# Kernel tuning notes

Measured on AMD Instinct MI355X. Metric: run time of the kernel, lower is better.

The kernel has to match this reference:

```python
import jax, jax.numpy as jnp
import numpy as np

H = 256          # LSTM hidden size
P = 1            # proj_size
L = 5            # num LSTM layers
T = 1000         # sequence length (forced by Linear(1000, 100))


def _uniform(key, shape, scale):
    return jax.random.uniform(key, shape, dtype=jnp.float32, minval=-scale, maxval=scale)


def setup_inputs() -> dict:
    key = jax.random.key(0)
    ks = jax.random.split(key, 16)
    B = 128
    s = 1.0 / np.sqrt(H)  # PyTorch LSTM init scale
    inp = {
        "x": jax.random.normal(ks[0], (B, T, 1), dtype=jnp.float32),
        # stacked LSTM params: layer input dim is 1 for all layers (input_size=1, proj_size=1)
        "Wih": _uniform(ks[1], (L, 4 * H, 1), s),
        "Whh": _uniform(ks[2], (L, 4 * H, P), s),
        "bih": _uniform(ks[3], (L, 4 * H), s),
        "bhh": _uniform(ks[4], (L, 4 * H), s),
        "Whr": _uniform(ks[5], (L, P, H), s),
        # MLP head
        "W1": _uniform(ks[6], (100, 1000), 1.0 / np.sqrt(1000)),
        "b1": _uniform(ks[7], (100,), 1.0 / np.sqrt(1000)),
        "W2": _uniform(ks[8], (100, 100), 0.1),
        "b2": _uniform(ks[9], (100,), 0.1),
        "W3": _uniform(ks[10], (100, 100), 0.1),
        "b3": _uniform(ks[11], (100,), 0.1),
        "W4": _uniform(ks[12], (1, 100), 0.1),
        "b4": _uniform(ks[13], (1,), 0.1),
    }
    return inp


def _lstm_layer(x_seq, Wih, Whh, bih, bhh, Whr):
    """One projected LSTM layer. x_seq: [B, T, in_dim] -> [B, T, P]."""
    B = x_seq.shape[0]
    # precompute input contribution for all timesteps: [B, T, 4H]
    gx = jnp.einsum('bti,gi->btg', x_seq, Wih) + bih + bhh
    gx = jnp.transpose(gx, (1, 0, 2))  # [T, B, 4H] for scan

    def step(carry, g_t):
        h, c = carry                      # h: [B, P], c: [B, H]
        gates = g_t + h @ Whh.T           # [B, 4H]
        i = jax.nn.sigmoid(gates[:, 0 * H:1 * H])
        f = jax.nn.sigmoid(gates[:, 1 * H:2 * H])
        g = jnp.tanh(gates[:, 2 * H:3 * H])
        o = jax.nn.sigmoid(gates[:, 3 * H:4 * H])
        c = f * c + i * g
        h = (o * jnp.tanh(c)) @ Whr.T     # projected hidden: [B, P]
        return (h, c), h

    h0 = jnp.zeros((B, P), x_seq.dtype)
    c0 = jnp.zeros((B, H), x_seq.dtype)
    _, hs = jax.lax.scan(step, (h0, c0), gx)  # hs: [T, B, P]
    return jnp.transpose(hs, (1, 0, 2))       # [B, T, P]


def reference(x, Wih, Whh, bih, bhh, Whr, W1, b1, W2, b2, W3, b3, W4, b4):
    out = x
    for l in range(L):  # fixed 5 stacked layers
        out = _lstm_layer(out, Wih[l], Whh[l], bih[l], bhh[l], Whr[l])
    out = out[:, :, 0]                      # squeeze -> [B, 1000]
    out = jax.nn.sigmoid(out @ W1.T + b1)   # linear1 + Sigmoid
    out = jax.nn.sigmoid(out @ W2.T + b2)   # linear2 + Sigmoid
    out = jax.nn.relu(out @ W3.T + b3)      # linear3 + ReLU
    out = out @ W4.T + b4                   # linear4 -> [B, 1]
    return out
```

## Files before the change

### kernel.cpp

```cpp
#include <hip/hip_runtime.h>


#define LAYERS 5
#define TT 1000
#define BATCH 128
#define CH 40
#define NCH (TT / CH)

__device__ __forceinline__ float fast_exp2(float x) {
#if __has_builtin(__builtin_amdgcn_exp2f)
  return __builtin_amdgcn_exp2f(x);
#else
  return __exp2f(x);
#endif
}
__device__ __forceinline__ float fast_rcp(float x) {
#if __has_builtin(__builtin_amdgcn_rcpf)
  return __builtin_amdgcn_rcpf(x);
#else
  return 1.0f / x;
#endif
}
__device__ __forceinline__ float fast_sigmoid(float z) {
  float e = fast_exp2(-1.4426950408889634f * z);
  return fast_rcp(1.0f + e);
}
__device__ __forceinline__ float fast_tanh(float z) {
  float e = fast_exp2(-2.8853900817779268f * z);
  return fmaf(2.0f, fast_rcp(1.0f + e), -1.0f);
}

template <int CTRL>
__device__ __forceinline__ float dpp_add(float v) {
  int moved = __builtin_amdgcn_update_dpp(0, __builtin_bit_cast(int, v),
                                          CTRL, 0xF, 0xF, false);
  return v + __builtin_bit_cast(float, moved);
}

__device__ __forceinline__ float wave_sum(float v) {
  v = dpp_add<0x128>(v);
  v = dpp_add<0x124>(v);
  v = dpp_add<0x122>(v);
  v = dpp_add<0x121>(v);
  int sw = __builtin_amdgcn_ds_swizzle(__builtin_bit_cast(int, v), 0x401F);
  v = v + __builtin_bit_cast(float, sw);
  float lo = __builtin_bit_cast(float, __builtin_amdgcn_readlane(__builtin_bit_cast(int, v), 0));
  float hi = __builtin_bit_cast(float, __builtin_amdgcn_readlane(__builtin_bit_cast(int, v), 32));
  return lo + hi;
}

__device__ __forceinline__ float lane_bcast(float v, int s) {
  return __builtin_bit_cast(float, __builtin_amdgcn_readlane(__builtin_bit_cast(int, v), s));
}

__global__ __launch_bounds__(64) void lstm_wave_kernel(
    const float* __restrict__ x,
    const float* __restrict__ Wih,
    const float* __restrict__ Whh,
    const float* __restrict__ bih,
    const float* __restrict__ bhh,
    const float* __restrict__ Whr,
    float* __restrict__ seq,
    int* __restrict__ flags)
{
  const int bid  = blockIdx.x;
  const int l    = bid >> 7;
  const int b    = bid & 127;
  const int lane = threadIdx.x;

  float wi[4][4], wh[4][4], bs[4][4], whr[4], cc[4];
  const int base = l * 1024;
#pragma unroll
  for (int g = 0; g < 4; ++g)
#pragma unroll
    for (int k = 0; k < 4; ++k) {
      int j = base + g * 256 + k * 64 + lane;
      wi[g][k] = Wih[j];
      wh[g][k] = Whh[j];
      bs[g][k] = bih[j] + bhh[j];
    }
#pragma unroll
  for (int k = 0; k < 4; ++k) {
    whr[k] = Whr[l * 256 + k * 64 + lane];
    cc[k] = 0.0f;
  }

  const float* in  = (l == 0) ? (x + b * TT) : (seq + ((l - 1) * BATCH + b) * TT);
  float*       out = seq + (l * BATCH + b) * TT;
  int*       my_flag = flags + l * BATCH + b;
  const int* in_flag = (l > 0) ? (flags + (l - 1) * BATCH + b) : (const int*)flags;

  float h = 0.0f;
  for (int c = 0; c < NCH; ++c) {
    if (l > 0) {
      while (__hip_atomic_load(in_flag, __ATOMIC_ACQUIRE,
                               __HIP_MEMORY_SCOPE_AGENT) <= c)
        __builtin_amdgcn_s_sleep(2);
    }
    float xv = 0.0f;
    if (lane < CH) {
      if (l == 0)
        xv = in[c * CH + lane];
      else
        xv = __hip_atomic_load(in + c * CH + lane, __ATOMIC_RELAXED,
                               __HIP_MEMORY_SCOPE_AGENT);
    }

    float outv = 0.0f;
    for (int s = 0; s < CH; ++s) {
      const float xs = lane_bcast(xv, s);
      float r = 0.0f;
#pragma unroll
      for (int k = 0; k < 4; ++k) {
        float pi = fmaf(xs, wi[0][k], fmaf(h, wh[0][k], bs[0][k]));
        float pf = fmaf(xs, wi[1][k], fmaf(h, wh[1][k], bs[1][k]));
        float pg = fmaf(xs, wi[2][k], fmaf(h, wh[2][k], bs[2][k]));
        float po = fmaf(xs, wi[3][k], fmaf(h, wh[3][k], bs[3][k]));
        float ig = fast_sigmoid(pi);
        float fg = fast_sigmoid(pf);
        float gg = fast_tanh(pg);
        float og = fast_sigmoid(po);
        cc[k] = fmaf(fg, cc[k], ig * gg);
        r += og * fast_tanh(cc[k]) * whr[k];
      }
      r = wave_sum(r);
      h = r;
      outv = (lane == s) ? r : outv;
    }

    if (l < 4) {
      if (lane < CH)
        __hip_atomic_store(out + c * CH + lane, outv, __ATOMIC_RELAXED,
                           __HIP_MEMORY_SCOPE_AGENT);
      if (lane == 0)
        __hip_atomic_store(my_flag, c + 1, __ATOMIC_RELEASE,
                           __HIP_MEMORY_SCOPE_AGENT);
    } else {
      if (lane < CH) out[c * CH + lane] = outv;
    }
  }
}

__global__ __launch_bounds__(128) void mlp_head_kernel(
    const float* __restrict__ seq4,
    const float* __restrict__ W1, const float* __restrict__ b1,
    const float* __restrict__ W2, const float* __restrict__ b2,
    const float* __restrict__ W3, const float* __restrict__ b3,
    const float* __restrict__ W4, const float* __restrict__ b4,
    float* __restrict__ out)
{
  __shared__ float sx[TT];
  __shared__ float sh[100];
  __shared__ float sh2[100];
  __shared__ float red[2];

  const int b = blockIdx.x, tid = threadIdx.x;
  for (int i = tid; i < TT; i += 128) sx[i] = seq4[b * TT + i];
  __syncthreads();

  if (tid < 100) {
    const float* w = W1 + tid * TT;
    float a0 = 0.f, a1 = 0.f, a2 = 0.f, a3 = 0.f;
    for (int t0 = 0; t0 < TT; t0 += 4) {
      float4 v = *(const float4*)(w + t0);
      a0 = fmaf(v.x, sx[t0 + 0], a0);
      a1 = fmaf(v.y, sx[t0 + 1], a1);
      a2 = fmaf(v.z, sx[t0 + 2], a2);
      a3 = fmaf(v.w, sx[t0 + 3], a3);
    }
    sh[tid] = fast_sigmoid((a0 + a1) + (a2 + a3) + b1[tid]);
  }
  __syncthreads();

  if (tid < 100) {
    float acc = b2[tid];
    const float* w = W2 + tid * 100;
    for (int k = 0; k < 100; ++k) acc += w[k] * sh[k];
    sh2[tid] = fast_sigmoid(acc);
  }
  __syncthreads();

  if (tid < 100) {
    float acc = b3[tid];
    const float* w = W3 + tid * 100;
    for (int k = 0; k < 100; ++k) acc += w[k] * sh2[k];
    sh[tid] = fmaxf(acc, 0.0f);
  }
  __syncthreads();

  float r = (tid < 100) ? sh[tid] * W4[tid] : 0.0f;
  {
    r = dpp_add<0x128>(r);
    r = dpp_add<0x124>(r);
    r = dpp_add<0x122>(r);
    r = dpp_add<0x121>(r);
    int sw = __builtin_amdgcn_ds_swizzle(__builtin_bit_cast(int, r), 0x401F);
    r = r + __builtin_bit_cast(float, sw);
    float lo = __builtin_bit_cast(float, __builtin_amdgcn_readlane(__builtin_bit_cast(int, r), 0));
    float hi = __builtin_bit_cast(float, __builtin_amdgcn_readlane(__builtin_bit_cast(int, r), 32));
    r = lo + hi;
  }
  if ((tid & 63) == 0) red[tid >> 6] = r;
  __syncthreads();
  if (tid == 0) out[b] = red[0] + red[1] + b4[0];
}

extern "C" void kernel_launch(void* const* d_in, const int* in_sizes, int n_in,
                              void* d_out, int out_size, void* d_ws, size_t ws_size,
                              hipStream_t stream) {
  const float* x   = (const float*)d_in[0];
  const float* Wih = (const float*)d_in[1];
  const float* Whh = (const float*)d_in[2];
  const float* bih = (const float*)d_in[3];
  const float* bhh = (const float*)d_in[4];
  const float* Whr = (const float*)d_in[5];
  const float* W1  = (const float*)d_in[6];
  const float* b1  = (const float*)d_in[7];
  const float* W2  = (const float*)d_in[8];
  const float* b2  = (const float*)d_in[9];
  const float* W3  = (const float*)d_in[10];
  const float* b3  = (const float*)d_in[11];
  const float* W4  = (const float*)d_in[12];
  const float* b4  = (const float*)d_in[13];

  float* seq   = (float*)d_ws;
  int*   flags = (int*)(seq + LAYERS * BATCH * TT);

  hipMemsetAsync(flags, 0, LAYERS * BATCH * sizeof(int), stream);
  lstm_wave_kernel<<<LAYERS * BATCH, 64, 0, stream>>>(x, Wih, Whh, bih, bhh, Whr,
                                                      seq, flags);
  mlp_head_kernel<<<BATCH, 128, 0, stream>>>(seq + 4 * BATCH * TT,
                                             W1, b1, W2, b2, W3, b3, W4, b4,
                                             (float*)d_out);
}
```

Measured before the change: 625.6 us.

## Shorten LSTM recurrence critical path and split MLP head dot product across threads

Gate weights and biases are pre-scaled by -log2(e) (and -2·log2(e) for the tanh gate), so each activation needs one fewer multiply. The input contribution xs*Wih+b is now computed apart from the h-dependent FMA, which keeps it off the serial recurrence chain. The wave reduction swaps ds_swizzle plus two readlanes for row_bcast DPP adds and one readlane, and the step loop is unrolled by 2. The MLP head uses 256 threads that split the 1000-long W1 dot product into two halves combined through shared memory; this is a minor cost compared with the serial LSTM kernel.

```diff
diff --git a/kernel.cpp b/kernel.cpp
--- a/kernel.cpp
+++ b/kernel.cpp
@@ -6,6 +6,8 @@
 #define BATCH 128
 #define CH 40
 #define NCH (TT / CH)
+
+#define LOG2E 1.4426950408889634f
 
 __device__ __forceinline__ float fast_exp2(float x) {
 #if __has_builtin(__builtin_amdgcn_exp2f)
@@ -22,12 +24,8 @@
 #endif
 }
 __device__ __forceinline__ float fast_sigmoid(float z) {
-  float e = fast_exp2(-1.4426950408889634f * z);
+  float e = fast_exp2(-LOG2E * z);
   return fast_rcp(1.0f + e);
-}
-__device__ __forceinline__ float fast_tanh(float z) {
-  float e = fast_exp2(-2.8853900817779268f * z);
-  return fmaf(2.0f, fast_rcp(1.0f + e), -1.0f);
 }
 
 template <int CTRL>
@@ -37,16 +35,14 @@
   return v + __builtin_bit_cast(float, moved);
 }
 
-__device__ __forceinline__ float wave_sum(float v) {
+__device__ __forceinline__ float wave_sum_uniform(float v) {
   v = dpp_add<0x128>(v);
   v = dpp_add<0x124>(v);
   v = dpp_add<0x122>(v);
   v = dpp_add<0x121>(v);
-  int sw = __builtin_amdgcn_ds_swizzle(__builtin_bit_cast(int, v), 0x401F);
-  v = v + __builtin_bit_cast(float, sw);
-  float lo = __builtin_bit_cast(float, __builtin_amdgcn_readlane(__builtin_bit_cast(int, v), 0));
-  float hi = __builtin_bit_cast(float, __builtin_amdgcn_readlane(__builtin_bit_cast(int, v), 32));
-  return lo + hi;
+  v = dpp_add<0x142>(v);
+  v = dpp_add<0x143>(v);
+  return __builtin_bit_cast(float, __builtin_amdgcn_readlane(__builtin_bit_cast(int, v), 63));
 }
 
 __device__ __forceinline__ float lane_bcast(float v, int s) {
@@ -68,17 +64,19 @@
   const int b    = bid & 127;
   const int lane = threadIdx.x;
 
-  float wi[4][4], wh[4][4], bs[4][4], whr[4], cc[4];
+  float wix[4][4], whx[4][4], gb[4][4], whr[4], cc[4];
   const int base = l * 1024;
 #pragma unroll
-  for (int g = 0; g < 4; ++g)
+  for (int g = 0; g < 4; ++g) {
+    const float sc = (g == 2) ? (-2.0f * LOG2E) : (-LOG2E);
 #pragma unroll
     for (int k = 0; k < 4; ++k) {
       int j = base + g * 256 + k * 64 + lane;
-      wi[g][k] = Wih[j];
-      wh[g][k] = Whh[j];
-      bs[g][k] = bih[j] + bhh[j];
-    }
+      wix[g][k] = Wih[j] * sc;
+      whx[g][k] = Whh[j] * sc;
+      gb[g][k]  = (bih[j] + bhh[j]) * sc;
+    }
+  }
 #pragma unroll
   for (int k = 0; k < 4; ++k) {
     whr[k] = Whr[l * 256 + k * 64 + lane];
@@ -107,25 +105,44 @@
     }
 
     float outv = 0.0f;
+#pragma unroll 2
     for (int s = 0; s < CH; ++s) {
       const float xs = lane_bcast(xv, s);
-      float r = 0.0f;
-#pragma unroll
-      for (int k = 0; k < 4; ++k) {
-        float pi = fmaf(xs, wi[0][k], fmaf(h, wh[0][k], bs[0][k]));
-        float pf = fmaf(xs, wi[1][k], fmaf(h, wh[1][k], bs[1][k]));
-        float pg = fmaf(xs, wi[2][k], fmaf(h, wh[2][k], bs[2][k]));
-        float po = fmaf(xs, wi[3][k], fmaf(h, wh[3][k], bs[3][k]));
-        float ig = fast_sigmoid(pi);
-        float fg = fast_sigmoid(pf);
-        float gg = fast_tanh(pg);
-        float og = fast_sigmoid(po);
-        cc[k] = fmaf(fg, cc[k], ig * gg);
-        r += og * fast_tanh(cc[k]) * whr[k];
+
+      float gx[4][4];
+#pragma unroll
+      for (int g = 0; g < 4; ++g)
+#pragma unroll
+        for (int k = 0; k < 4; ++k)
+          gx[g][k] = fmaf(xs, wix[g][k], gb[g][k]);
+
+      float E[4][4];
+#pragma unroll
+      for (int g = 0; g < 4; ++g)
+#pragma unroll
+        for (int k = 0; k < 4; ++k)
+          E[g][k] = fast_exp2(fmaf(h, whx[g][k], gx[g][k]));
+
+      float r0, r1, r2, r3;
+      {
+        float rr[4];
+#pragma unroll
+        for (int k = 0; k < 4; ++k) {
+          float ig = fast_rcp(1.0f + E[0][k]);
+          float fg = fast_rcp(1.0f + E[1][k]);
+          float gg = fmaf(2.0f, fast_rcp(1.0f + E[2][k]), -1.0f);
+          float og = fast_rcp(1.0f + E[3][k]);
+          cc[k] = fmaf(fg, cc[k], ig * gg);
+          float tE = fast_exp2(cc[k] * (-2.0f * LOG2E));
+          float tc = fmaf(2.0f, fast_rcp(1.0f + tE), -1.0f);
+          rr[k] = og * tc * whr[k];
+        }
+        r0 = rr[0]; r1 = rr[1]; r2 = rr[2]; r3 = rr[3];
       }
-      r = wave_sum(r);
-      h = r;
-      outv = (lane == s) ? r : outv;
+      float r = (r0 + r1) + (r2 + r3);
+
+      h = wave_sum_uniform(r);
+      if (lane == s) outv = h;
     }
 
     if (l < 4) {
@@ -141,7 +158,7 @@
   }
 }
 
-__global__ __launch_bounds__(128) void mlp_head_kernel(
+__global__ __launch_bounds__(256) void mlp_head_kernel(
     const float* __restrict__ seq4,
     const float* __restrict__ W1, const float* __restrict__ b1,
     const float* __restrict__ W2, const float* __restrict__ b2,
@@ -152,24 +169,32 @@
   __shared__ float sx[TT];
   __shared__ float sh[100];
   __shared__ float sh2[100];
-  __shared__ float red[2];
+  __shared__ float part[100];
+  __shared__ float red[4];
 
   const int b = blockIdx.x, tid = threadIdx.x;
-  for (int i = tid; i < TT; i += 128) sx[i] = seq4[b * TT + i];
-  __syncthreads();
-
-  if (tid < 100) {
-    const float* w = W1 + tid * TT;
+  for (int i = tid; i < TT; i += 256) sx[i] = seq4[b * TT + i];
+  __syncthreads();
+
+  const int half = (tid >= 128) ? 1 : 0;
+  const int oid  = half ? (tid - 128) : tid;
+  float myacc = 0.0f;
+  if (oid < 100) {
+    const float* w  = W1 + oid * TT + half * 500;
+    const float* xx = sx + half * 500;
     float a0 = 0.f, a1 = 0.f, a2 = 0.f, a3 = 0.f;
-    for (int t0 = 0; t0 < TT; t0 += 4) {
+    for (int t0 = 0; t0 < 500; t0 += 4) {
       float4 v = *(const float4*)(w + t0);
-      a0 = fmaf(v.x, sx[t0 + 0], a0);
-      a1 = fmaf(v.y, sx[t0 + 1], a1);
-      a2 = fmaf(v.z, sx[t0 + 2], a2);
-      a3 = fmaf(v.w, sx[t0 + 3], a3);
-    }
-    sh[tid] = fast_sigmoid((a0 + a1) + (a2 + a3) + b1[tid]);
-  }
+      a0 = fmaf(v.x, xx[t0 + 0], a0);
+      a1 = fmaf(v.y, xx[t0 + 1], a1);
+      a2 = fmaf(v.z, xx[t0 + 2], a2);
+      a3 = fmaf(v.w, xx[t0 + 3], a3);
+    }
+    myacc = (a0 + a1) + (a2 + a3);
+    if (half) part[oid] = myacc;
+  }
+  __syncthreads();
+  if (tid < 100) sh[tid] = fast_sigmoid(myacc + part[tid] + b1[tid]);
   __syncthreads();
 
   if (tid < 100) {
@@ -194,15 +219,13 @@
     r = dpp_add<0x124>(r);
     r = dpp_add<0x122>(r);
     r = dpp_add<0x121>(r);
-    int sw = __builtin_amdgcn_ds_swizzle(__builtin_bit_cast(int, r), 0x401F);
-    r = r + __builtin_bit_cast(float, sw);
-    float lo = __builtin_bit_cast(float, __builtin_amdgcn_readlane(__builtin_bit_cast(int, r), 0));
-    float hi = __builtin_bit_cast(float, __builtin_amdgcn_readlane(__builtin_bit_cast(int, r), 32));
-    r = lo + hi;
+    r = dpp_add<0x142>(r);
+    r = dpp_add<0x143>(r);
+    r = __builtin_bit_cast(float, __builtin_amdgcn_readlane(__builtin_bit_cast(int, r), 63));
   }
   if ((tid & 63) == 0) red[tid >> 6] = r;
   __syncthreads();
-  if (tid == 0) out[b] = red[0] + red[1] + b4[0];
+  if (tid == 0) out[b] = (red[0] + red[1]) + (red[2] + red[3]) + b4[0];
 }
 
 extern "C" void kernel_launch(void* const* d_in, const int* in_sizes, int n_in,
@@ -229,7 +252,7 @@
   hipMemsetAsync(flags, 0, LAYERS * BATCH * sizeof(int), stream);
   lstm_wave_kernel<<<LAYERS * BATCH, 64, 0, stream>>>(x, Wih, Whh, bih, bhh, Whr,
                                                       seq, flags);
-  mlp_head_kernel<<<BATCH, 128, 0, stream>>>(seq + 4 * BATCH * TT,
+  mlp_head_kernel<<<BATCH, 256, 0, stream>>>(seq + 4 * BATCH * TT,
                                              W1, b1, W2, b2, W3, b3, W4, b4,
                                              (float*)d_out);
 }
```

New measurement: 558.1 us. 1.12x faster.
